# Kernel tuning notes

Measured on AMD Instinct MI355X. Metric: run time of the kernel, lower is better.

Reference implementation:

```python
import jax, jax.numpy as jnp
import numpy as np

M, K = 4096, 4096
ORDER = 12  # ceil(log2(max(M,K)))
BATCH, SEQ = 4, 2048


def _hilbert_d_grid(order, m, k):
    """Vectorized xy->d Hilbert-curve index for an m x k grid (numpy, int)."""
    n = 1 << order
    ii, jj = np.meshgrid(np.arange(m, dtype=np.int64), np.arange(k, dtype=np.int64), indexing='ij')
    x, y = jj.copy(), ii.copy()
    d = np.zeros_like(x)
    s = n >> 1
    while s > 0:
        rx = ((x & s) > 0).astype(np.int64)
        ry = ((y & s) > 0).astype(np.int64)
        d += s * s * ((3 * rx) ^ ry)
        # rotate quadrant
        swap = ry == 0
        flip = swap & (rx == 1)
        xf = np.where(flip, s - 1 - x, x)
        yf = np.where(flip, s - 1 - y, y)
        x = np.where(swap, yf, xf)
        y = np.where(swap, xf, yf)
        s >>= 1
    return d.astype(np.int32)


def setup_inputs() -> dict:
    key = jax.random.key(0)
    k1, = jax.random.split(key, 1)
    x = jax.random.normal(k1, (BATCH, SEQ, K), dtype=jnp.float32)
    # dna init per __init__: [4.0,1.0,1.0,0.5,0.5,0.5] with dna[0] += (seed%100)/10 for seed=42
    dna = jnp.array([8.2, 1.0, 1.0, 0.5, 0.5, 0.5], dtype=jnp.float32)
    bias = jnp.zeros((M,), dtype=jnp.float32)
    hilbert_d = jnp.asarray(_hilbert_d_grid(ORDER, M, K))  # [M, K] int32
    return {"x": x, "dna": dna, "bias": bias, "hilbert_d": hilbert_d}


def reference(x, dna, bias, hilbert_d):
    # dna is detached in the torch forward (weights built from numpy copy)
    p = jax.lax.stop_gradient(dna)
    m_p, a, b, n1, n2, n3 = p[0], p[1], p[2], p[3], p[4], p[5]
    total = jnp.float32((1 << ORDER) * (1 << ORDER))
    theta = hilbert_d.astype(jnp.float32) * (2.0 * jnp.pi / total)  # [M,K]
    ang = m_p * theta * 0.25
    base = jnp.abs(jnp.cos(ang) / a) ** n2 + jnp.abs(jnp.sin(ang) / b) ** n3
    r = base ** (-1.0 / n1)  # Gielis superformula radius, [M,K]
    w = (r - r.mean()) / (jnp.std(r, ddof=1) + 1e-9)  # torch .std() is unbiased
    scale = jnp.float32(1.0 / np.sqrt(K))
    return jnp.einsum('bsk,mk->bsm', x, w) * scale + bias
```

## Files before the change

kernel.cpp:

```cpp
#include <hip/hip_runtime.h>

#define M_DIM 4096
#define K_DIM 4096
#define NR_DIM 8192
#define TOTAL_ELEMS (M_DIM * K_DIM)

typedef unsigned short u16;
typedef unsigned int u32;
typedef __bf16 bf16x8 __attribute__((ext_vector_type(8)));
typedef float f32x4 __attribute__((ext_vector_type(4)));
typedef u16 u16x8 __attribute__((ext_vector_type(8)));

__device__ __forceinline__ u16 f2b(float f) {
    u32 v;
    __builtin_memcpy(&v, &f, sizeof(v));
    v += 0x7FFFu + ((v >> 16) & 1u);
    return (u16)(v >> 16);
}

__device__ __forceinline__ void abs_sincos(float ang, float* s, float* c) {
    float q = rintf(ang * 0.636619772f);
    float r1 = fmaf(q, -1.57079637e+00f, ang);
    float r = fmaf(q, 4.37113883e-08f, r1);
    float r2 = r * r;
    float ts = fmaf(r2, -1.9840874e-04f, 8.3333310e-03f);
    ts = fmaf(r2, ts, -1.6666667e-01f);
    float sp = fmaf(r * r2, ts, r);
    float tc = fmaf(r2, -1.3888378e-03f, 4.1666638e-02f);
    tc = fmaf(r2, tc, -5.0e-01f);
    float cp = fmaf(r2, tc, 1.0f);
    bool sw = (((int)q) & 1) != 0;
    *s = sw ? cp : sp;
    *c = sw ? sp : cp;
}

__device__ __forceinline__ float compute_r_fast(int d, float c_ang) {
    float s, c;
    abs_sincos((float)d * c_ang, &s, &c);
    float base = __builtin_amdgcn_sqrtf(fabsf(c)) + __builtin_amdgcn_sqrtf(fabsf(s));
    return __builtin_amdgcn_rcpf(base * base);
}

__device__ __noinline__ float compute_r_gen(int d, float c_ang, float inv_a,
                                            float inv_b, float n2, float n3, float e) {
    float s, c;
    abs_sincos((float)d * c_ang, &s, &c);
    float ca = fabsf(c) * fabsf(inv_a);
    float sb = fabsf(s) * fabsf(inv_b);
    float t1 = (n2 == 0.5f) ? sqrtf(ca) : ((n2 == 1.0f) ? ca : powf(ca, n2));
    float t2 = (n3 == 0.5f) ? sqrtf(sb) : ((n3 == 1.0f) ? sb : powf(sb, n3));
    float base = t1 + t2;
    if (e == -2.0f) { float ib = __builtin_amdgcn_rcpf(base); return ib * ib; }
    if (e == -1.0f) return __builtin_amdgcn_rcpf(base);
    return powf(base, e);
}

__device__ __forceinline__ bool dna_is_fast(const float* p) {
    return (p[1] == 1.0f) & (p[2] == 1.0f) & (p[3] == 0.5f) &
           (p[4] == 0.5f) & (p[5] == 0.5f);
}

__global__ void __launch_bounds__(256) reduce_kernel(const float* __restrict__ dna,
                                                     double* __restrict__ sums) {
    float p[6];
#pragma unroll
    for (int i = 0; i < 6; i++) p[i] = dna[i];
    float c_ang = (float)((double)p[0] * 6.283185307179586 / 67108864.0);

    double s = 0.0, s2 = 0.0;
    int idx = blockIdx.x * blockDim.x + threadIdx.x;
    int stride = gridDim.x * blockDim.x;
    if (dna_is_fast(p)) {
        for (int d = idx; d < TOTAL_ELEMS; d += stride) {
            float r = compute_r_fast(d, c_ang);
            s += (double)r;
            s2 += (double)r * (double)r;
        }
    } else {
        float inv_a = 1.0f / p[1], inv_b = 1.0f / p[2], e = -1.0f / p[3];
        for (int d = idx; d < TOTAL_ELEMS; d += stride) {
            float r = compute_r_gen(d, c_ang, inv_a, inv_b, p[4], p[5], e);
            s += (double)r;
            s2 += (double)r * (double)r;
        }
    }
#pragma unroll
    for (int off = 32; off > 0; off >>= 1) {
        s += __shfl_down(s, off);
        s2 += __shfl_down(s2, off);
    }
    __shared__ double ls[4], ls2[4];
    int lane = threadIdx.x & 63, w = threadIdx.x >> 6;
    if (lane == 0) { ls[w] = s; ls2[w] = s2; }
    __syncthreads();
    if (threadIdx.x == 0) {
        atomicAdd(&sums[0], ls[0] + ls[1] + ls[2] + ls[3]);
        atomicAdd(&sums[1], ls2[0] + ls2[1] + ls2[2] + ls2[3]);
    }
}

__global__ void __launch_bounds__(256) build_w_kernel(const int* __restrict__ hd,
                                                      const float* __restrict__ dna,
                                                      const double* __restrict__ sums,
                                                      u16* __restrict__ W) {
    float p[6];
#pragma unroll
    for (int i = 0; i < 6; i++) p[i] = dna[i];
    float c_ang = (float)((double)p[0] * 6.283185307179586 / 67108864.0);

    const double cnt = (double)TOTAL_ELEMS;
    double sum = sums[0], sumsq = sums[1];
    float meanf = (float)(sum / cnt);
    float stdf = (float)sqrt((sumsq - sum * sum / cnt) / (cnt - 1.0));
    float sc = 0.015625f / (stdf + 1e-9f);

    int idx = blockIdx.x * blockDim.x + threadIdx.x;
    int stride = gridDim.x * blockDim.x;
    if (dna_is_fast(p)) {
        for (int i = idx * 4; i < TOTAL_ELEMS; i += stride * 4) {
            int4 d4 = *(const int4*)(hd + i);
            ushort4 o;
            o.x = f2b((compute_r_fast(d4.x, c_ang) - meanf) * sc);
            o.y = f2b((compute_r_fast(d4.y, c_ang) - meanf) * sc);
            o.z = f2b((compute_r_fast(d4.z, c_ang) - meanf) * sc);
            o.w = f2b((compute_r_fast(d4.w, c_ang) - meanf) * sc);
            *(ushort4*)(W + i) = o;
        }
    } else {
        float inv_a = 1.0f / p[1], inv_b = 1.0f / p[2], e = -1.0f / p[3];
        for (int i = idx * 4; i < TOTAL_ELEMS; i += stride * 4) {
            int4 d4 = *(const int4*)(hd + i);
            ushort4 o;
            o.x = f2b((compute_r_gen(d4.x, c_ang, inv_a, inv_b, p[4], p[5], e) - meanf) * sc);
            o.y = f2b((compute_r_gen(d4.y, c_ang, inv_a, inv_b, p[4], p[5], e) - meanf) * sc);
            o.z = f2b((compute_r_gen(d4.z, c_ang, inv_a, inv_b, p[4], p[5], e) - meanf) * sc);
            o.w = f2b((compute_r_gen(d4.w, c_ang, inv_a, inv_b, p[4], p[5], e) - meanf) * sc);
            *(ushort4*)(W + i) = o;
        }
    }
}

__global__ void __launch_bounds__(256) convert_x_kernel(const float* __restrict__ x,
                                                        u16* __restrict__ xb) {
    int i = (blockIdx.x * blockDim.x + threadIdx.x) * 8;
    const float4* xv = (const float4*)(x + i);
    float4 a = xv[0], b = xv[1];
    u16x8 o;
    o[0] = f2b(a.x); o[1] = f2b(a.y); o[2] = f2b(a.z); o[3] = f2b(a.w);
    o[4] = f2b(b.x); o[5] = f2b(b.y); o[6] = f2b(b.z); o[7] = f2b(b.w);
    *(u16x8*)(xb + i) = o;
}

#define BM 256
#define BN 256
#define BK 64

__device__ __forceinline__ void gld_lds16(const u16* g, u16* l) {
    __builtin_amdgcn_global_load_lds(
        (const __attribute__((address_space(1))) void*)g,
        (__attribute__((address_space(3))) void*)l,
        16, 0, 0);
}

#define FENCE asm volatile("" ::: "memory")
#define WAIT_VM6 asm volatile("s_waitcnt vmcnt(6)" ::: "memory")
#define WAIT_VM4 asm volatile("s_waitcnt vmcnt(4)" ::: "memory")
#define SB0 __builtin_amdgcn_sched_barrier(0)

#define ISSUE_A(dst, bufv, ks, h)                                             \
    _Pragma("unroll") for (int m = 0; m < 4; ++m) {                           \
        int row = wr * 128 + ((h) * 4 + m) * 16 + lrow;                       \
        dst[m] = *(const bf16x8*)(&sA[bufv][ks][row * 32 + oA]);              \
    }

#define ISSUE_B(dst, bufv, ks)                                                \
    _Pragma("unroll") for (int n = 0; n < 4; ++n) {                           \
        int row = wc * 64 + n * 16 + lrow;                                    \
        dst[n] = *(const bf16x8*)(&sB[bufv][ks][row * 32 + oA]);              \
    }

#define MFMA_HALF(h, afb, bfb)                                                \
    __builtin_amdgcn_s_setprio(1);                                            \
    _Pragma("unroll") for (int m = 0; m < 4; ++m)                             \
        _Pragma("unroll") for (int n = 0; n < 4; ++n)                         \
            acc[(h) * 4 + m][n] = __builtin_amdgcn_mfma_f32_16x16x32_bf16(    \
                afb[m], bfb[n], acc[(h) * 4 + m][n], 0, 0, 0);                \
    __builtin_amdgcn_s_setprio(0)

__global__ void __launch_bounds__(512, 2) gemm_kernel(const u16* __restrict__ A,
                                                      const u16* __restrict__ B,
                                                      const float* __restrict__ bias,
                                                      float* __restrict__ C) {
    __shared__ __align__(16) u16 sA[2][2][BM * 32];
    __shared__ __align__(16) u16 sB[2][2][BN * 32];

    const int tid = threadIdx.x;
    const int lane = tid & 63;
    const int wave = tid >> 6;
    const int wr = wave >> 2;
    const int wc = wave & 3;
    const int lrow = lane & 15;
    const int lq = lane >> 4;
    const int oA = ((lq ^ ((lrow >> 1) & 3)) << 3);

    const int flat = blockIdx.y * 16 + blockIdx.x;
    const int swz = (flat & 7) * 64 + (flat >> 3);
    const int bx = swz & 15;
    const int by = swz >> 4;
    const int i0 = by * BM;
    const int j0 = bx * BN;

    const int srow0 = tid >> 2;
    const int olog = (tid & 3) ^ ((srow0 >> 1) & 3);
    const int aoff0 = (i0 + srow0) * K_DIM + olog * 8;
    const int aoff1 = aoff0 + 128 * K_DIM;
    const int boff0 = (j0 + srow0) * K_DIM + olog * 8;
    const int boff1 = boff0 + 128 * K_DIM;
    const int lds_l0 = tid * 8;
    const int lds_l1 = (tid + 512) * 8;

    auto stage = [&](const u16* base, int off0, int off1, u16* slot, int kb) {
        gld_lds16(base + off0 + kb, slot + lds_l0);
        gld_lds16(base + off1 + kb, slot + lds_l1);
    };

    const f32x4 vzero = {0.f, 0.f, 0.f, 0.f};
    f32x4 acc[8][4];
#pragma unroll
    for (int a = 0; a < 8; a++)
#pragma unroll
        for (int b = 0; b < 4; b++) acc[a][b] = vzero;

    stage(A, aoff0, aoff1, sA[0][0], 0);
    stage(B, boff0, boff1, sB[0][0], 0);
    stage(A, aoff0, aoff1, sA[0][1], 32);
    stage(B, boff0, boff1, sB[0][1], 32);
    stage(A, aoff0, aoff1, sA[1][0], 64);
    stage(B, boff0, boff1, sB[1][0], 64);
    WAIT_VM4;
    FENCE;
    __builtin_amdgcn_s_barrier();

    bf16x8 afA[4], afB[4], bfA[4], bfB[4];
    ISSUE_A(afA, 0, 0, 0);
    ISSUE_B(bfA, 0, 0);
    FENCE;

    for (int kt = 0; kt < K_DIM / BK; ++kt) {
        const int bufv = kt & 1;
        const int kb1 = (kt + 1 < 64 ? kt + 1 : 63) * 64 + 32;
        const int kb2 = (kt + 2 < 64 ? kt + 2 : 63) * 64;

        ISSUE_A(afB, bufv, 0, 1);
        stage(A, aoff0, aoff1, sA[bufv ^ 1][1], kb1);
        SB0;
        MFMA_HALF(0, afA, bfA);
        WAIT_VM6;
        FENCE;
        __builtin_amdgcn_s_barrier();

        ISSUE_A(afA, bufv, 1, 0);
        ISSUE_B(bfB, bufv, 1);
        stage(B, boff0, boff1, sB[bufv ^ 1][1], kb1);
        SB0;
        MFMA_HALF(1, afB, bfA);
        FENCE;
        __builtin_amdgcn_s_barrier();

        ISSUE_A(afB, bufv, 1, 1);
        stage(A, aoff0, aoff1, sA[bufv][0], kb2);
        SB0;
        MFMA_HALF(0, afA, bfB);
        WAIT_VM6;
        FENCE;
        __builtin_amdgcn_s_barrier();

        ISSUE_A(afA, bufv ^ 1, 0, 0);
        ISSUE_B(bfA, bufv ^ 1, 0);
        stage(B, boff0, boff1, sB[bufv][0], kb2);
        SB0;
        MFMA_HALF(1, afB, bfB);
        FENCE;
        __builtin_amdgcn_s_barrier();
    }

#pragma unroll
    for (int ni = 0; ni < 4; ++ni) {
        long j = j0 + wc * 64 + ni * 16 + lrow;
        float bv = bias[j];
#pragma unroll
        for (int mi = 0; mi < 8; ++mi) {
            long ib = i0 + wr * 128 + mi * 16 + lq * 4;
#pragma unroll
            for (int r = 0; r < 4; ++r) {
                C[(ib + r) * M_DIM + j] = acc[mi][ni][r] + bv;
            }
        }
    }
}

extern "C" void kernel_launch(void* const* d_in, const int* in_sizes, int n_in,
                              void* d_out, int out_size, void* d_ws, size_t ws_size,
                              hipStream_t stream) {
    const float* x = (const float*)d_in[0];
    const float* dna = (const float*)d_in[1];
    const float* bias = (const float*)d_in[2];
    const int* hd = (const int*)d_in[3];
    float* out = (float*)d_out;

    double* sums = (double*)d_ws;
    u16* W = (u16*)((char*)d_ws + 256);
    u16* Xb = (u16*)((char*)d_ws + 256 + (size_t)TOTAL_ELEMS * 2);

    hipMemsetAsync(d_ws, 0, 256, stream);
    reduce_kernel<<<dim3(1024), dim3(256), 0, stream>>>(dna, sums);
    build_w_kernel<<<dim3(2048), dim3(256), 0, stream>>>(hd, dna, sums, W);
    convert_x_kernel<<<dim3((NR_DIM * K_DIM) / (256 * 8)), dim3(256), 0, stream>>>(x, Xb);
    gemm_kernel<<<dim3(M_DIM / BN, NR_DIM / BM), dim3(512), 0, stream>>>(Xb, W, bias, out);
}
```

Baseline: 574.9 us.

## Restructure GEMM main loop into two phases with larger register fragment prefetch

```diff
diff --git a/kernel.cpp b/kernel.cpp
--- a/kernel.cpp
+++ b/kernel.cpp
@@ -163,7 +163,6 @@
 }
 
 #define FENCE asm volatile("" ::: "memory")
-#define WAIT_VM6 asm volatile("s_waitcnt vmcnt(6)" ::: "memory")
 #define WAIT_VM4 asm volatile("s_waitcnt vmcnt(4)" ::: "memory")
 #define SB0 __builtin_amdgcn_sched_barrier(0)
 
@@ -180,12 +179,10 @@
     }
 
 #define MFMA_HALF(h, afb, bfb)                                                \
-    __builtin_amdgcn_s_setprio(1);                                            \
     _Pragma("unroll") for (int m = 0; m < 4; ++m)                             \
         _Pragma("unroll") for (int n = 0; n < 4; ++n)                         \
             acc[(h) * 4 + m][n] = __builtin_amdgcn_mfma_f32_16x16x32_bf16(    \
-                afb[m], bfb[n], acc[(h) * 4 + m][n], 0, 0, 0);                \
-    __builtin_amdgcn_s_setprio(0)
+                afb[m], bfb[n], acc[(h) * 4 + m][n], 0, 0, 0)
 
 __global__ void __launch_bounds__(512, 2) gemm_kernel(const u16* __restrict__ A,
                                                       const u16* __restrict__ B,
@@ -241,45 +238,42 @@
     FENCE;
     __builtin_amdgcn_s_barrier();
 
-    bf16x8 afA[4], afB[4], bfA[4], bfB[4];
+    bf16x8 afA[4], afB[4], afC[4], afD[4], bfA[4], bfB[4];
     ISSUE_A(afA, 0, 0, 0);
+    ISSUE_A(afB, 0, 0, 1);
     ISSUE_B(bfA, 0, 0);
     FENCE;
 
     for (int kt = 0; kt < K_DIM / BK; ++kt) {
-        const int bufv = kt & 1;
+        const int p = kt & 1;
         const int kb1 = (kt + 1 < 64 ? kt + 1 : 63) * 64 + 32;
         const int kb2 = (kt + 2 < 64 ? kt + 2 : 63) * 64;
 
-        ISSUE_A(afB, bufv, 0, 1);
-        stage(A, aoff0, aoff1, sA[bufv ^ 1][1], kb1);
+        ISSUE_A(afC, p, 1, 0);
+        ISSUE_A(afD, p, 1, 1);
+        ISSUE_B(bfB, p, 1);
+        stage(A, aoff0, aoff1, sA[p ^ 1][1], kb1);
+        stage(B, boff0, boff1, sB[p ^ 1][1], kb1);
         SB0;
+        __builtin_amdgcn_s_setprio(1);
         MFMA_HALF(0, afA, bfA);
-        WAIT_VM6;
+        MFMA_HALF(1, afB, bfA);
+        __builtin_amdgcn_s_setprio(0);
+        WAIT_VM4;
         FENCE;
         __builtin_amdgcn_s_barrier();
 
-        ISSUE_A(afA, bufv, 1, 0);
-        ISSUE_B(bfB, bufv, 1);
-        stage(B, boff0, boff1, sB[bufv ^ 1][1], kb1);
+        ISSUE_A(afA, p ^ 1, 0, 0);
+        ISSUE_A(afB, p ^ 1, 0, 1);
+        ISSUE_B(bfA, p ^ 1, 0);
+        stage(A, aoff0, aoff1, sA[p][0], kb2);
+        stage(B, boff0, boff1, sB[p][0], kb2);
         SB0;
-        MFMA_HALF(1, afB, bfA);
-        FENCE;
-        __builtin_amdgcn_s_barrier();
-
-        ISSUE_A(afB, bufv, 1, 1);
-        stage(A, aoff0, aoff1, sA[bufv][0], kb2);
-        SB0;
-        MFMA_HALF(0, afA, bfB);
-        WAIT_VM6;
-        FENCE;
-        __builtin_amdgcn_s_barrier();
-
-        ISSUE_A(afA, bufv ^ 1, 0, 0);
-        ISSUE_B(bfA, bufv ^ 1, 0);
-        stage(B, boff0, boff1, sB[bufv][0], kb2);
-        SB0;
-        MFMA_HALF(1, afB, bfB);
+        __builtin_amdgcn_s_setprio(1);
+        MFMA_HALF(0, afC, bfB);
+        MFMA_HALF(1, afD, bfB);
+        __builtin_amdgcn_s_setprio(0);
+        WAIT_VM4;
         FENCE;
         __builtin_amdgcn_s_barrier();
     }
```

After: 539.8 us. 1.06x faster.
